# Optimization experiments

Hardware: AMD Instinct MI355X
Metric: run time of the kernel (lower is better)

Reference implementation:

```python
import jax, jax.numpy as jnp
import numpy as np


def setup_inputs() -> dict:
    key = jax.random.key(0)
    kq, kk, kv, km = jax.random.split(key, 4)
    B, H, N, D = 2, 16, 2048, 64
    q = jax.random.normal(kq, (B, H, N, D), dtype=jnp.float32)
    k = jax.random.normal(kk, (B, H, N, D), dtype=jnp.float32)
    v = jax.random.normal(kv, (B, H, N, D), dtype=jnp.float32)
    # mask > 0 (True) means the key position is masked OUT (matches masked_fill semantics)
    mask = jax.random.randint(km, (B, N), 0, 2).astype(bool)
    return {"q": q, "k": k, "v": v, "mask": mask}


def reference(q, k, v, mask):
    # q, k, v: [b, h, n, d]; mask: [b, n] (True = masked out)
    scale = q.shape[-1] ** -0.5
    sim = jnp.einsum('bhid,bhjd->bhij', q, k) * scale
    # L2-distance score: 2*q.k - |q|^2 - |k|^2 (scaled dot already includes `scale`)
    q_sq = jnp.sum(q ** 2, axis=-1, keepdims=True)            # [b, h, n, 1]
    k_sq = jnp.sum(k ** 2, axis=-1, keepdims=True).swapaxes(-1, -2)  # [b, h, 1, n]
    sim = sim * 2 - q_sq - k_sq
    neg_max = -jnp.finfo(sim.dtype).max
    sim = jnp.where(mask[:, None, None, :], neg_max, sim)
    attn = jax.nn.softmax(sim, axis=-1)
    out = jnp.einsum('bhij,bhjd->bhid', attn, v)
    return out
```

## Files before the change

kernel.cpp:

```cpp
#include <hip/hip_runtime.h>

#define B_ 2
#define H_ 16
#define N_ 2048
#define D_ 64
#define NH_ (B_*H_)
#define ROWS_ (NH_*N_)
#define KVB 64
#define NT (N_/KVB)
#define LOG2E 1.4426950408889634f
#define QSCALE (0.25f * LOG2E)

typedef _Float16 f16;
typedef _Float16 f16x2 __attribute__((ext_vector_type(2)));
typedef _Float16 f16x4 __attribute__((ext_vector_type(4)));
typedef _Float16 f16x8 __attribute__((ext_vector_type(8)));
typedef __fp16 h16x2 __attribute__((ext_vector_type(2)));
typedef float f32x4 __attribute__((ext_vector_type(4)));

typedef __attribute__((address_space(1))) const void g_void;
typedef __attribute__((address_space(3))) void l_void;

__device__ __forceinline__ void gl_lds16(const void* g, void* l) {
  __builtin_amdgcn_global_load_lds((g_void*)g, (l_void*)l, 16, 0, 0);
}

__device__ __forceinline__ f16x2 cvt_pk(float a, float b) {
  return __builtin_bit_cast(f16x2, __builtin_amdgcn_cvt_pkrtz(a, b));
}

__device__ __forceinline__ float dot2acc(f16x2 a, f16x2 b, float c) {
#if __has_builtin(__builtin_amdgcn_fdot2)
  return __builtin_amdgcn_fdot2(__builtin_bit_cast(h16x2, a),
                                __builtin_bit_cast(h16x2, b), c, false);
#else
  return c + (float)a[0] * (float)b[0] + (float)a[1] * (float)b[1];
#endif
}

__global__ __launch_bounds__(256) void prep_all(
    const float* __restrict__ q, const float* __restrict__ k,
    const float* __restrict__ v, const void* __restrict__ mask,
    f16* __restrict__ qh, f16* __restrict__ kh, f16* __restrict__ vt,
    float* __restrict__ bias) {
  int tid = threadIdx.x;
  if (blockIdx.x < 1024) {
    int head = blockIdx.x >> 5;
    int n0 = (blockIdx.x & 31) << 6;
    int e = tid & 15, gq = tid >> 4;
    const float* src = v + ((long)head * N_ + n0 + e * 4) * D_ + gq * 4;
    f32x4 r0 = *(const f32x4*)(src);
    f32x4 r1 = *(const f32x4*)(src + D_);
    f32x4 r2 = *(const f32x4*)(src + 2 * D_);
    f32x4 r3 = *(const f32x4*)(src + 3 * D_);
    f16* dst = vt + (long)head * D_ * N_ + n0 + e * 4;
#pragma unroll
    for (int c = 0; c < 4; ++c) {
      f16x4 y;
      y[0] = (f16)r0[c]; y[1] = (f16)r1[c]; y[2] = (f16)r2[c]; y[3] = (f16)r3[c];
      *(f16x4*)(dst + (long)(gq * 4 + c) * N_) = y;
    }
  } else {
    int wid = (blockIdx.x - 1024) * 4 + (tid >> 6);
    int lane = tid & 63;
    int r8 = lane >> 3, e = lane & 7;
    const unsigned* mw = (const unsigned*)mask;
    bool bytes_mode = __any(mw[lane] > 1u);
#pragma unroll
    for (int trip = 0; trip < 4; ++trip) {
      long grow = ((long)(trip * 4096 + wid)) * 8 + r8;
      bool isK = grow >= ROWS_;
      long row = isK ? grow - ROWS_ : grow;
      const float* s = (isK ? k : q) + row * D_ + e * 8;
      f32x4 x0 = *(const f32x4*)s;
      f32x4 x1 = *(const f32x4*)(s + 4);
      float scl = isK ? 1.0f : QSCALE;
      f16x8 hv;
#pragma unroll
      for (int c = 0; c < 4; ++c) { hv[c] = (f16)(x0[c] * scl); hv[4 + c] = (f16)(x1[c] * scl); }
      *(f16x8*)((isK ? kh : qh) + row * D_ + e * 8) = hv;
      if (isK) {
        float sq = x0[0]*x0[0] + x0[1]*x0[1] + x0[2]*x0[2] + x0[3]*x0[3]
                 + x1[0]*x1[0] + x1[1]*x1[1] + x1[2]*x1[2] + x1[3]*x1[3];
        sq += __shfl_xor(sq, 1); sq += __shfl_xor(sq, 2); sq += __shfl_xor(sq, 4);
        if (e == 0) {
          int b = (int)(row >> 15);
          int n = (int)(row & (N_ - 1));
          int mv = bytes_mode ? (int)((const unsigned char*)mask)[b * N_ + n]
                              : ((const int*)mask)[b * N_ + n];
          bias[row] = mv ? -1e30f : -sq * LOG2E;
        }
      }
    }
  }
}

__global__ __launch_bounds__(256, 4) void attend_main(
    const f16* __restrict__ qh, const f16* __restrict__ kh,
    const f16* __restrict__ vt, const float* __restrict__ bias,
    float* __restrict__ out) {
  __shared__ f16 Kt[2][4096];
  __shared__ f16 Vt[2][4096];
  __shared__ f16 Pb[4][1024];

  int tid = threadIdx.x;
  int w = tid >> 6, lane = tid & 63;
  int j = lane & 15, g = lane >> 4;

  int bid = (blockIdx.x & 7) * 128 + (blockIdx.x >> 3);
  int head = bid >> 5;
  int qt = bid & 31;
  int qrow0 = qt * 64 + w * 16;
  int off = ((bid >> 5) & 3) * 8;

  const f16* qbase = qh + ((long)head * N_ + qrow0 + j) * D_;
  f16x8 qf0 = *(const f16x8*)(qbase + g * 8);
  f16x8 qf1 = *(const f16x8*)(qbase + 32 + g * 8);

  const char* kg = (const char*)(kh + (long)head * N_ * D_);
  const char* vg = (const char*)(vt + (long)head * D_ * N_);
  const float* bb = bias + (long)head * N_ + g * 4;

  int ko0[4], ko1[4];
#pragma unroll
  for (int x = 0; x < 4; ++x) {
    int rk = x * 16 + j;
    int swk = (rk & 7) << 4;
    ko0[x] = ((rk << 7) + g * 16) ^ swk;
    ko1[x] = ((rk << 7) + 64 + g * 16) ^ swk;
  }
  int pswz = (j & 7) << 4;
  int pw0 = ((j << 7) + g * 8) ^ pswz;
  int pr0 = ((j << 7) + g * 16) ^ pswz;
  int pr1 = ((j << 7) + 64 + g * 16) ^ pswz;

  f32x4 O0 = {0.f,0.f,0.f,0.f}, O1 = {0.f,0.f,0.f,0.f};
  f32x4 O2 = {0.f,0.f,0.f,0.f}, O3 = {0.f,0.f,0.f,0.f};
  float m = -1e30f, l = 0.f;

  auto stage = [&](int buf, int t) {
    int kv = t * KVB;
    if (w < 2) {
      const char* src = kg + (size_t)kv * 128;
      char* lb = (char*)&Kt[buf][0];
#pragma unroll
      for (int c = 0; c < 4; ++c) {
        int chunk = w * 4 + c;
        int o = chunk * 1024 + lane * 16;
        int p = o ^ (((o >> 7) & 7) << 4);
        gl_lds16(src + p, lb + chunk * 1024);
      }
    } else {
      const char* src = vg + (size_t)kv * 2;
      char* lb = (char*)&Vt[buf][0];
#pragma unroll
      for (int c = 0; c < 4; ++c) {
        int chunk = (w - 2) * 4 + c;
        int o = chunk * 1024 + lane * 16;
        int p = o ^ (((o >> 7) & 7) << 4);
        gl_lds16(src + (size_t)(p >> 7) * (N_ * 2) + (p & 127), lb + chunk * 1024);
      }
    }
  };

  f32x4 bnx[4];
#pragma unroll
  for (int jt = 0; jt < 4; ++jt) bnx[jt] = *(const f32x4*)(bb + off * KVB + jt * 16);

  stage(0, off);
  __syncthreads();
  int cur = 0;

  for (int t = 0; t < NT; ++t) {
    int tt = (t + off) & (NT - 1);
    int tn = (tt + 1) & (NT - 1);
    if (t + 1 < NT) stage(cur ^ 1, tn);

    const char* Kc = (const char*)&Kt[cur][0];
    const char* Vc = (const char*)&Vt[cur][0];

    f32x4 sA[4];
    __builtin_amdgcn_s_setprio(1);
#pragma unroll
    for (int jt = 0; jt < 4; ++jt) {
      f16x8 k0 = *(const f16x8*)(Kc + ko0[jt]);
      f16x8 k1 = *(const f16x8*)(Kc + ko1[jt]);
      f32x4 a = __builtin_amdgcn_mfma_f32_16x16x32_f16(k0, qf0, bnx[jt], 0, 0, 0);
      sA[jt]  = __builtin_amdgcn_mfma_f32_16x16x32_f16(k1, qf1, a, 0, 0, 0);
    }
    __builtin_amdgcn_s_setprio(0);

    if (t + 1 < NT) {
#pragma unroll
      for (int jt = 0; jt < 4; ++jt)
        bnx[jt] = *(const f32x4*)(bb + tn * KVB + jt * 16);
    }

    float tm;
    {
      float a0 = fmaxf(fmaxf(sA[0][0], sA[0][1]), fmaxf(sA[0][2], sA[0][3]));
      float a1 = fmaxf(fmaxf(sA[1][0], sA[1][1]), fmaxf(sA[1][2], sA[1][3]));
      float a2 = fmaxf(fmaxf(sA[2][0], sA[2][1]), fmaxf(sA[2][2], sA[2][3]));
      float a3 = fmaxf(fmaxf(sA[3][0], sA[3][1]), fmaxf(sA[3][2], sA[3][3]));
      tm = fmaxf(fmaxf(a0, a1), fmaxf(a2, a3));
    }
    tm = fmaxf(tm, __shfl_xor(tm, 16));
    tm = fmaxf(tm, __shfl_xor(tm, 32));

    bool fastok = (tm - m <= 8.0f) && (m > -1e29f);
    if (!__all(fastok)) {
      float mn = fmaxf(m, tm);
      float sc = __builtin_amdgcn_exp2f(m - mn);
      m = mn;
      l *= sc;
#pragma unroll
      for (int r = 0; r < 4; ++r) {
        float scr = __shfl(sc, g * 4 + r);
        O0[r] *= scr; O1[r] *= scr; O2[r] *= scr; O3[r] *= scr;
      }
    }

    f16x2 pk[8];
    float rsum = 0.f;
    const f16x2 ones = {(f16)1.0f, (f16)1.0f};
#pragma unroll
    for (int jt = 0; jt < 4; ++jt) {
      float p0 = __builtin_amdgcn_exp2f(sA[jt][0] - m);
      float p1 = __builtin_amdgcn_exp2f(sA[jt][1] - m);
      float p2 = __builtin_amdgcn_exp2f(sA[jt][2] - m);
      float p3 = __builtin_amdgcn_exp2f(sA[jt][3] - m);
      pk[jt * 2 + 0] = cvt_pk(p0, p1);
      pk[jt * 2 + 1] = cvt_pk(p2, p3);
      rsum = dot2acc(pk[jt * 2 + 0], ones, rsum);
      rsum = dot2acc(pk[jt * 2 + 1], ones, rsum);
    }
    rsum += __shfl_xor(rsum, 16);
    rsum += __shfl_xor(rsum, 32);
    l += rsum;

    char* Pw = (char*)&Pb[w][0];
#pragma unroll
    for (int jt = 0; jt < 4; ++jt) {
      f16x4 pv_ = __builtin_shufflevector(pk[jt * 2], pk[jt * 2 + 1], 0, 1, 2, 3);
      *(f16x4*)(Pw + (pw0 ^ (jt * 32))) = pv_;
    }
    f16x8 pf0 = *(const f16x8*)(Pw + pr0);
    f16x8 pf1 = *(const f16x8*)(Pw + pr1);

    __builtin_amdgcn_s_setprio(1);
#pragma unroll
    for (int dt = 0; dt < 4; ++dt) {
      f16x8 v0 = *(const f16x8*)(Vc + ko0[dt]);
      f16x8 v1 = *(const f16x8*)(Vc + ko1[dt]);
      f32x4* Od = (dt == 0) ? &O0 : (dt == 1) ? &O1 : (dt == 2) ? &O2 : &O3;
      *Od = __builtin_amdgcn_mfma_f32_16x16x32_f16(pf0, v0, *Od, 0, 0, 0);
      *Od = __builtin_amdgcn_mfma_f32_16x16x32_f16(pf1, v1, *Od, 0, 0, 0);
    }
    __builtin_amdgcn_s_setprio(0);

    __syncthreads();
    cur ^= 1;
  }

  float* ob = out + ((long)head * N_ + qrow0 + g * 4) * D_ + j;
#pragma unroll
  for (int r = 0; r < 4; ++r) {
    float inv = 1.0f / __shfl(l, g * 4 + r);
    float* o2 = ob + (long)r * D_;
    o2[0]  = O0[r] * inv;
    o2[16] = O1[r] * inv;
    o2[32] = O2[r] * inv;
    o2[48] = O3[r] * inv;
  }
}

extern "C" void kernel_launch(void* const* d_in, const int* in_sizes, int n_in,
                              void* d_out, int out_size, void* d_ws, size_t ws_size,
                              hipStream_t stream) {
  const float* q = (const float*)d_in[0];
  const float* k = (const float*)d_in[1];
  const float* v = (const float*)d_in[2];
  const void* mask = d_in[3];

  char* ws = (char*)d_ws;
  f16*   qh   = (f16*)ws;
  f16*   kh   = (f16*)(ws + (8u  << 20));
  f16*   vt   = (f16*)(ws + (16u << 20));
  float* bias = (float*)(ws + (24u << 20));
  float* out  = (float*)d_out;

  prep_all<<<dim3(2048), dim3(256), 0, stream>>>(q, k, v, mask, qh, kh, vt, bias);
  attend_main<<<dim3(NH_ * (N_ / 64)), dim3(256), 0, stream>>>(qh, kh, vt, bias, out);
}
```

Before: 155.2 us.

## Fold running max into MFMA accumulator bias and defer row-sum reduction

The first KV tile is peeled to initialise the running max. After that, the current max is subtracted from the per-key bias that seeds the QK^T MFMA accumulator, so the scores come out already shifted and the per-element subtraction before exp2 disappears. The per-tile max shuffle reduction now runs only when some lane exceeds the threshold, and the row-sum cross-lane shuffles move out of the loop to a single reduction at the end. This cuts VALU and cross-lane work on the softmax path, at the cost of extra code size and a bias-adjustment step each iteration.

```diff
diff --git a/kernel.cpp b/kernel.cpp
--- a/kernel.cpp
+++ b/kernel.cpp
@@ -163,81 +163,33 @@
     }
   };
 
-  f32x4 bnx[4];
-#pragma unroll
-  for (int jt = 0; jt < 4; ++jt) bnx[jt] = *(const f32x4*)(bb + off * KVB + jt * 16);
-
-  stage(0, off);
-  __syncthreads();
-  int cur = 0;
-
-  for (int t = 0; t < NT; ++t) {
-    int tt = (t + off) & (NT - 1);
-    int tn = (tt + 1) & (NT - 1);
-    if (t + 1 < NT) stage(cur ^ 1, tn);
-
-    const char* Kc = (const char*)&Kt[cur][0];
-    const char* Vc = (const char*)&Vt[cur][0];
-
-    f32x4 sA[4];
+  auto qkt = [&](const char* Kc, f32x4* sA, const f32x4* cin) {
     __builtin_amdgcn_s_setprio(1);
 #pragma unroll
     for (int jt = 0; jt < 4; ++jt) {
       f16x8 k0 = *(const f16x8*)(Kc + ko0[jt]);
       f16x8 k1 = *(const f16x8*)(Kc + ko1[jt]);
-      f32x4 a = __builtin_amdgcn_mfma_f32_16x16x32_f16(k0, qf0, bnx[jt], 0, 0, 0);
+      f32x4 a = __builtin_amdgcn_mfma_f32_16x16x32_f16(k0, qf0, cin[jt], 0, 0, 0);
       sA[jt]  = __builtin_amdgcn_mfma_f32_16x16x32_f16(k1, qf1, a, 0, 0, 0);
     }
     __builtin_amdgcn_s_setprio(0);
-
-    if (t + 1 < NT) {
-#pragma unroll
-      for (int jt = 0; jt < 4; ++jt)
-        bnx[jt] = *(const f32x4*)(bb + tn * KVB + jt * 16);
-    }
-
-    float tm;
-    {
-      float a0 = fmaxf(fmaxf(sA[0][0], sA[0][1]), fmaxf(sA[0][2], sA[0][3]));
-      float a1 = fmaxf(fmaxf(sA[1][0], sA[1][1]), fmaxf(sA[1][2], sA[1][3]));
-      float a2 = fmaxf(fmaxf(sA[2][0], sA[2][1]), fmaxf(sA[2][2], sA[2][3]));
-      float a3 = fmaxf(fmaxf(sA[3][0], sA[3][1]), fmaxf(sA[3][2], sA[3][3]));
-      tm = fmaxf(fmaxf(a0, a1), fmaxf(a2, a3));
-    }
-    tm = fmaxf(tm, __shfl_xor(tm, 16));
-    tm = fmaxf(tm, __shfl_xor(tm, 32));
-
-    bool fastok = (tm - m <= 8.0f) && (m > -1e29f);
-    if (!__all(fastok)) {
-      float mn = fmaxf(m, tm);
-      float sc = __builtin_amdgcn_exp2f(m - mn);
-      m = mn;
-      l *= sc;
-#pragma unroll
-      for (int r = 0; r < 4; ++r) {
-        float scr = __shfl(sc, g * 4 + r);
-        O0[r] *= scr; O1[r] *= scr; O2[r] *= scr; O3[r] *= scr;
-      }
-    }
-
+  };
+  auto finish_pv = [&](const char* Vc, const f32x4* sA) {
     f16x2 pk[8];
     float rsum = 0.f;
     const f16x2 ones = {(f16)1.0f, (f16)1.0f};
 #pragma unroll
     for (int jt = 0; jt < 4; ++jt) {
-      float p0 = __builtin_amdgcn_exp2f(sA[jt][0] - m);
-      float p1 = __builtin_amdgcn_exp2f(sA[jt][1] - m);
-      float p2 = __builtin_amdgcn_exp2f(sA[jt][2] - m);
-      float p3 = __builtin_amdgcn_exp2f(sA[jt][3] - m);
+      float p0 = __builtin_amdgcn_exp2f(sA[jt][0]);
+      float p1 = __builtin_amdgcn_exp2f(sA[jt][1]);
+      float p2 = __builtin_amdgcn_exp2f(sA[jt][2]);
+      float p3 = __builtin_amdgcn_exp2f(sA[jt][3]);
       pk[jt * 2 + 0] = cvt_pk(p0, p1);
       pk[jt * 2 + 1] = cvt_pk(p2, p3);
       rsum = dot2acc(pk[jt * 2 + 0], ones, rsum);
       rsum = dot2acc(pk[jt * 2 + 1], ones, rsum);
     }
-    rsum += __shfl_xor(rsum, 16);
-    rsum += __shfl_xor(rsum, 32);
     l += rsum;
-
     char* Pw = (char*)&Pb[w][0];
 #pragma unroll
     for (int jt = 0; jt < 4; ++jt) {
@@ -246,7 +198,6 @@
     }
     f16x8 pf0 = *(const f16x8*)(Pw + pr0);
     f16x8 pf1 = *(const f16x8*)(Pw + pr1);
-
     __builtin_amdgcn_s_setprio(1);
 #pragma unroll
     for (int dt = 0; dt < 4; ++dt) {
@@ -257,11 +208,91 @@
       *Od = __builtin_amdgcn_mfma_f32_16x16x32_f16(pf1, v1, *Od, 0, 0, 0);
     }
     __builtin_amdgcn_s_setprio(0);
-
+  };
+  auto lane_max16 = [&](const f32x4* sA) {
+    float a0 = fmaxf(fmaxf(sA[0][0], sA[0][1]), fmaxf(sA[0][2], sA[0][3]));
+    float a1 = fmaxf(fmaxf(sA[1][0], sA[1][1]), fmaxf(sA[1][2], sA[1][3]));
+    float a2 = fmaxf(fmaxf(sA[2][0], sA[2][1]), fmaxf(sA[2][2], sA[2][3]));
+    float a3 = fmaxf(fmaxf(sA[3][0], sA[3][1]), fmaxf(sA[3][2], sA[3][3]));
+    return fmaxf(fmaxf(a0, a1), fmaxf(a2, a3));
+  };
+
+  f32x4 bnx[4];
+#pragma unroll
+  for (int jt = 0; jt < 4; ++jt) bnx[jt] = *(const f32x4*)(bb + off * KVB + jt * 16);
+
+  stage(0, off);
+  __syncthreads();
+  int cur = 0;
+
+  {
+    int tn = (off + 1) & (NT - 1);
+    stage(1, tn);
+    f32x4 sA[4];
+    qkt((const char*)&Kt[0][0], sA, bnx);
+#pragma unroll
+    for (int jt = 0; jt < 4; ++jt) bnx[jt] = *(const f32x4*)(bb + tn * KVB + jt * 16);
+
+    float tm = lane_max16(sA);
+    tm = fmaxf(tm, __shfl_xor(tm, 16));
+    tm = fmaxf(tm, __shfl_xor(tm, 32));
+    m = fmaxf(m, tm);
+#pragma unroll
+    for (int jt = 0; jt < 4; ++jt)
+#pragma unroll
+      for (int r = 0; r < 4; ++r) sA[jt][r] -= m;
+    finish_pv((const char*)&Vt[0][0], sA);
+    __syncthreads();
+    cur = 1;
+  }
+
+  for (int t = 1; t < NT; ++t) {
+    int tt = (t + off) & (NT - 1);
+    int tn = (tt + 1) & (NT - 1);
+
+    f32x4 madj[4];
+#pragma unroll
+    for (int jt = 0; jt < 4; ++jt) {
+      madj[jt][0] = bnx[jt][0] - m; madj[jt][1] = bnx[jt][1] - m;
+      madj[jt][2] = bnx[jt][2] - m; madj[jt][3] = bnx[jt][3] - m;
+    }
+    if (t + 1 < NT) stage(cur ^ 1, tn);
+
+    f32x4 sA[4];
+    qkt((const char*)&Kt[cur][0], sA, madj);
+
+    if (t + 1 < NT) {
+#pragma unroll
+      for (int jt = 0; jt < 4; ++jt)
+        bnx[jt] = *(const f32x4*)(bb + tn * KVB + jt * 16);
+    }
+
+    float tmL = lane_max16(sA);
+    if (!__all(tmL <= 8.0f)) {
+      float tmr = fmaxf(tmL, __shfl_xor(tmL, 16));
+      tmr = fmaxf(tmr, __shfl_xor(tmr, 32));
+      float delta = fmaxf(tmr, 0.0f);
+      float sc = __builtin_amdgcn_exp2f(-delta);
+      m += delta;
+      l *= sc;
+#pragma unroll
+      for (int r = 0; r < 4; ++r) {
+        float scr = __shfl(sc, g * 4 + r);
+        O0[r] *= scr; O1[r] *= scr; O2[r] *= scr; O3[r] *= scr;
+      }
+#pragma unroll
+      for (int jt = 0; jt < 4; ++jt)
+#pragma unroll
+        for (int r = 0; r < 4; ++r) sA[jt][r] -= delta;
+    }
+
+    finish_pv((const char*)&Vt[cur][0], sA);
     __syncthreads();
     cur ^= 1;
   }
 
+  l += __shfl_xor(l, 16);
+  l += __shfl_xor(l, 32);
   float* ob = out + ((long)head * N_ + qrow0 + g * 4) * D_ + j;
 #pragma unroll
   for (int r = 0; r < 4; ++r) {
```

Measured after the change: 151.1 us. -2.6%, faster.
